# Performance work log

Hardware: AMD Instinct MI355X
Metric: run time of the kernel (lower is better)

Reference implementation:

```python
import jax, jax.numpy as jnp
import numpy as np


def setup_inputs() -> dict:
    key = jax.random.key(0)
    ks = jax.random.split(key, 12)
    B, T, S, H, I = 32, 32, 400, 1024, 1024
    s = 0.02  # weight init scale
    return {
        "input_": jax.random.normal(ks[0], (B, T, I), jnp.float32),
        "h0": jax.random.normal(ks[1], (B, H), jnp.float32),
        "c0": jax.random.normal(ks[2], (B, H), jnp.float32),
        "h_attn0": jax.random.normal(ks[3], (B, H), jnp.float32),
        "encoder_hy": jax.random.normal(ks[4], (S, B, H), jnp.float32),
        "past_attn": jax.random.uniform(ks[5], (B, S), jnp.float32),
        "W_ih": jax.random.normal(ks[6], (4 * H, I + H), jnp.float32) * s,
        "W_hh": jax.random.normal(ks[7], (4 * H, H), jnp.float32) * s,
        "b_ih": jnp.zeros((4 * H,), jnp.float32),
        "b_hh": jnp.zeros((4 * H,), jnp.float32),
        "W_attn": jax.random.normal(ks[8], (H, H), jnp.float32) * s,
        "W_out": jax.random.normal(ks[9], (H, 2 * H), jnp.float32) * s,
    }


def _decode(input_, h0, c0, h_attn0, encoder_hy, W_ih, W_hh, b_ih, b_hh, W_attn, W_out):
    # encoder_hy: [S, B, H] -> enhy: [B, S, H]
    enhy = jnp.transpose(encoder_hy, (1, 0, 2))
    # attn_in(enhy) is time-invariant (linear, fixed enhy): hoist out of the loop
    enhy_new = jnp.einsum("bsh,gh->bsg", enhy, W_attn)  # [B, S, H]
    xs = jnp.transpose(input_, (1, 0, 2))  # [T, B, I] (batch_first)

    def step(carry, x_k):
        h, c, h_attn = carry
        x = jnp.concatenate([x_k, h_attn], axis=1)  # [B, I+H]
        gates = x @ W_ih.T + b_ih + h @ W_hh.T + b_hh  # [B, 4H]
        i, f, g, o = jnp.split(gates, 4, axis=1)  # torch LSTMCell gate order
        i = jax.nn.sigmoid(i)
        f = jax.nn.sigmoid(f)
        g = jnp.tanh(g)
        o = jax.nn.sigmoid(o)
        c = f * c + i * g
        h = o * jnp.tanh(c)
        # luong_general: attn = bmm(attn_in(enhy), dehy)
        attn = jax.nn.softmax(jnp.einsum("bsh,bh->bs", enhy_new, h), axis=1)
        ctx = jnp.einsum("bs,bsh->bh", attn, enhy)
        h_attn = jnp.tanh(jnp.concatenate([ctx, h], axis=1) @ W_out.T)
        return (h, c, h_attn), (h_attn, attn)

    (h, c, h_attn), (outs, attns) = jax.lax.scan(step, (h0, c0, h_attn0), xs)
    output = jnp.transpose(outs, (1, 0, 2))  # [B, T, H] (batch_first)
    return output, h, c, h_attn, attns  # attns: [T, B, S]


def reference(input_, h0, c0, h_attn0, encoder_hy, past_attn,
              W_ih, W_hh, b_ih, b_hh, W_attn, W_out):
    output, h, c, h_attn, out_attn = _decode(
        input_, h0, c0, h_attn0, encoder_hy, W_ih, W_hh, b_ih, b_hh, W_attn, W_out)
    # coverage='none': past_attn passes through unchanged; loss_cv stays 0.0
    return output, h, c, h_attn, out_attn, past_attn, jnp.float32(0.0)
```

## Files before the change

### kernel.cpp

```cpp
#include <hip/hip_runtime.h>
#include <hip/hip_bf16.h>

using u16 = unsigned short;
typedef __attribute__((ext_vector_type(8))) short bf16x8;
typedef __attribute__((ext_vector_type(4))) float f32x4;
typedef __attribute__((ext_vector_type(4))) u16 u16x4;


__device__ __forceinline__ float bf2f(u16 u){ union{unsigned int i; float f;} v; v.i = ((unsigned int)u)<<16; return v.f; }
__device__ __forceinline__ u16 f2bf(float f){ __hip_bfloat16 h = __float2bfloat16(f); return *reinterpret_cast<u16*>(&h); }
struct HL { u16 h, l; };
__device__ __forceinline__ HL split1(float f){
  HL r; r.h = f2bf(f); r.l = f2bf(f - bf2f(r.h)); return r;
}
__device__ __forceinline__ f32x4 mfma16(bf16x8 a, bf16x8 b, f32x4 c){ return __builtin_amdgcn_mfma_f32_16x16x32_bf16(a,b,c,0,0,0); }


__global__ __launch_bounds__(256) void cast_wih_k(const float* __restrict__ Wih,
    u16* __restrict__ Wxh, u16* __restrict__ Wxl, u16* __restrict__ Wrh, u16* __restrict__ Wrl){
  int v = blockIdx.x*256 + threadIdx.x;
  if (v >= (4096*2048)/4) return;
  int flat = v*4; int j = flat >> 11; int k = flat & 2047;
  float4 f = *(const float4*)(Wih + flat);
  HL s0 = split1(f.x), s1 = split1(f.y), s2 = split1(f.z), s3 = split1(f.w);
  u16x4 h, l;
  h[0]=s0.h; h[1]=s1.h; h[2]=s2.h; h[3]=s3.h;
  l[0]=s0.l; l[1]=s1.l; l[2]=s2.l; l[3]=s3.l;
  if (k < 1024){
    *(u16x4*)(Wxh + (size_t)j*1024 + k) = h;
    *(u16x4*)(Wxl + (size_t)j*1024 + k) = l;
  } else {
    *(u16x4*)(Wrh + (size_t)j*2048 + (k-1024)) = h;
    *(u16x4*)(Wrl + (size_t)j*2048 + (k-1024)) = l;
  }
}

__global__ __launch_bounds__(256) void cast_whh_k(const float* __restrict__ Whh,
    u16* __restrict__ Wrh, u16* __restrict__ Wrl){
  int v = blockIdx.x*256 + threadIdx.x;
  if (v >= (4096*1024)/4) return;
  int flat = v*4; int j = flat >> 10; int k = flat & 1023;
  float4 f = *(const float4*)(Whh + flat);
  HL s0 = split1(f.x), s1 = split1(f.y), s2 = split1(f.z), s3 = split1(f.w);
  u16x4 h, l;
  h[0]=s0.h; h[1]=s1.h; h[2]=s2.h; h[3]=s3.h;
  l[0]=s0.l; l[1]=s1.l; l[2]=s2.l; l[3]=s3.l;
  *(u16x4*)(Wrh + (size_t)j*2048 + 1024 + k) = h;
  *(u16x4*)(Wrl + (size_t)j*2048 + 1024 + k) = l;
}

__global__ __launch_bounds__(256) void cast_split_k(const float* __restrict__ src,
    u16* __restrict__ dh, u16* __restrict__ dl, int n4){
  int v = blockIdx.x*256 + threadIdx.x;
  if (v >= n4) return;
  float4 f = *(const float4*)(src + (size_t)v*4);
  HL s0 = split1(f.x), s1 = split1(f.y), s2 = split1(f.z), s3 = split1(f.w);
  u16x4 h, l;
  h[0]=s0.h; h[1]=s1.h; h[2]=s2.h; h[3]=s3.h;
  l[0]=s0.l; l[1]=s1.l; l[2]=s2.l; l[3]=s3.l;
  *(u16x4*)(dh + (size_t)v*4) = h;
  *(u16x4*)(dl + (size_t)v*4) = l;
}

__global__ __launch_bounds__(256) void cast_x_k(const float* __restrict__ inp,
    u16* __restrict__ Xh, u16* __restrict__ Xl){
  int v = blockIdx.x*256 + threadIdx.x;
  if (v >= (1024*1024)/4) return;
  int flat = v*4; int m = flat >> 10; int k = flat & 1023;
  int t = m >> 5, b = m & 31;
  float4 f = *(const float4*)(inp + ((size_t)(b*32 + t) << 10) + k);
  HL s0 = split1(f.x), s1 = split1(f.y), s2 = split1(f.z), s3 = split1(f.w);
  u16x4 h, l;
  h[0]=s0.h; h[1]=s1.h; h[2]=s2.h; h[3]=s3.h;
  l[0]=s0.l; l[1]=s1.l; l[2]=s2.l; l[3]=s3.l;
  *(u16x4*)(Xh + flat) = h;
  *(u16x4*)(Xl + flat) = l;
}

__global__ __launch_bounds__(256) void watsplit_k(const float* __restrict__ Wattn,
    u16* __restrict__ Wth, u16* __restrict__ Wtl){
  __shared__ float t[32][33];
  int gx = blockIdx.x, cx = blockIdx.y;
  int ty = threadIdx.x >> 5, tx = threadIdx.x & 31;
  #pragma unroll
  for (int i=0;i<4;++i){
    int g = gx*32 + ty + i*8;
    t[ty+i*8][tx] = Wattn[(size_t)g*1024 + cx*32 + tx];
  }
  __syncthreads();
  #pragma unroll
  for (int i=0;i<4;++i){
    int c = cx*32 + ty + i*8;
    HL s = split1(t[tx][ty+i*8]);
    Wth[(size_t)c*1024 + gx*32 + tx] = s.h;
    Wtl[(size_t)c*1024 + gx*32 + tx] = s.l;
  }
}

__global__ __launch_bounds__(256) void init_misc_k(const float* __restrict__ h0, const float* __restrict__ c0,
    const float* __restrict__ ha0, const float* __restrict__ past,
    u16* __restrict__ Zh0, u16* __restrict__ Zl0, float* __restrict__ cbuf,
    float* __restrict__ out_past, float* __restrict__ out_loss){
  int idx = blockIdx.x*256 + threadIdx.x;
  if (idx < 65536){
    int b = idx >> 11, col = idx & 2047;
    float v = (col < 1024) ? ha0[b*1024 + col] : h0[b*1024 + col - 1024];
    HL s = split1(v);
    Zh0[idx] = s.h; Zl0[idx] = s.l;
  } else if (idx < 65536 + 32768){
    int i = idx - 65536; cbuf[i] = c0[i];
  } else if (idx < 65536 + 32768 + 12800){
    int i = idx - 98304; out_past[i] = past[i];
  } else if (idx == 65536 + 32768 + 12800){
    out_loss[0] = 0.f;
  }
}

__global__ __launch_bounds__(256) void gemm128_bias_k(
    const u16* __restrict__ Ah, const u16* __restrict__ Al,
    const u16* __restrict__ Bh, const u16* __restrict__ Bl, float* __restrict__ C,
    const float* __restrict__ bias0, const float* __restrict__ bias1, int M, int N, int K)
{
  __shared__ __align__(16) u16 Ash[4096], Asl[4096], Bsh[4096], Bsl[4096];
  const int tid = threadIdx.x;
  const int lane = tid & 63, w = tid >> 6;
  const int wm = w >> 1, wn = w & 1;
  const int m0 = blockIdx.y * 128, n0 = blockIdx.x * 128;
  const int r = lane & 15, q = lane >> 4;

  f32x4 acc[4][4];
  #pragma unroll
  for (int i=0;i<4;i++)
    #pragma unroll
    for (int j=0;j<4;j++) acc[i][j] = (f32x4){0.f,0.f,0.f,0.f};

  const int NT = K >> 5;
  const int srow = tid >> 2;
  const int skp  = (tid & 3) * 8;
  bf16x8 rah0, rah1, ral0, ral1, rbh0, rbh1, rbl0, rbl1;

  {
    size_t ao = (size_t)(m0 + srow) * K + skp;
    size_t bo = (size_t)(n0 + srow) * K + skp;
    rah0 = *(const bf16x8*)(Ah + ao);  rah1 = *(const bf16x8*)(Ah + ao + (size_t)64*K);
    ral0 = *(const bf16x8*)(Al + ao);  ral1 = *(const bf16x8*)(Al + ao + (size_t)64*K);
    rbh0 = *(const bf16x8*)(Bh + bo);  rbh1 = *(const bf16x8*)(Bh + bo + (size_t)64*K);
    rbl0 = *(const bf16x8*)(Bl + bo);  rbl1 = *(const bf16x8*)(Bl + bo + (size_t)64*K);
  }

  for (int kt = 0; kt < NT; ++kt){
    __syncthreads();
    *(bf16x8*)(Ash + tid*8)        = rah0;
    *(bf16x8*)(Ash + 2048 + tid*8) = rah1;
    *(bf16x8*)(Asl + tid*8)        = ral0;
    *(bf16x8*)(Asl + 2048 + tid*8) = ral1;
    *(bf16x8*)(Bsh + tid*8)        = rbh0;
    *(bf16x8*)(Bsh + 2048 + tid*8) = rbh1;
    *(bf16x8*)(Bsl + tid*8)        = rbl0;
    *(bf16x8*)(Bsl + 2048 + tid*8) = rbl1;
    __syncthreads();
    if (kt + 1 < NT){
      size_t ao = (size_t)(m0 + srow) * K + (kt+1)*32 + skp;
      size_t bo = (size_t)(n0 + srow) * K + (kt+1)*32 + skp;
      rah0 = *(const bf16x8*)(Ah + ao);  rah1 = *(const bf16x8*)(Ah + ao + (size_t)64*K);
      ral0 = *(const bf16x8*)(Al + ao);  ral1 = *(const bf16x8*)(Al + ao + (size_t)64*K);
      rbh0 = *(const bf16x8*)(Bh + bo);  rbh1 = *(const bf16x8*)(Bh + bo + (size_t)64*K);
      rbl0 = *(const bf16x8*)(Bl + bo);  rbl1 = *(const bf16x8*)(Bl + bo + (size_t)64*K);
    }
    bf16x8 afh[4], afl[4], bfh[4], bfl[4];
    #pragma unroll
    for (int mf=0; mf<4; ++mf){
      int off = (wm*64 + mf*16 + r)*32 + q*8;
      afh[mf] = *(const bf16x8*)(Ash + off);
      afl[mf] = *(const bf16x8*)(Asl + off);
    }
    #pragma unroll
    for (int nf=0; nf<4; ++nf){
      int off = (wn*64 + nf*16 + r)*32 + q*8;
      bfh[nf] = *(const bf16x8*)(Bsh + off);
      bfl[nf] = *(const bf16x8*)(Bsl + off);
    }
    #pragma unroll
    for (int mf=0; mf<4; ++mf)
      #pragma unroll
      for (int nf=0; nf<4; ++nf){
        acc[mf][nf] = mfma16(afh[mf], bfh[nf], acc[mf][nf]);
        acc[mf][nf] = mfma16(afh[mf], bfl[nf], acc[mf][nf]);
        acc[mf][nf] = mfma16(afl[mf], bfh[nf], acc[mf][nf]);
      }
  }

  #pragma unroll
  for (int mf=0; mf<4; ++mf)
    #pragma unroll
    for (int nf=0; nf<4; ++nf)
      #pragma unroll
      for (int rr=0; rr<4; ++rr){
        int row = m0 + wm*64 + mf*16 + q*4 + rr;
        int col = n0 + wn*64 + nf*16 + r;
        C[(size_t)row*N + col] = acc[mf][nf][rr] + bias0[col] + bias1[col];
      }
}


__global__ __launch_bounds__(512) void rec_partial_k(
    const u16* __restrict__ Zh, const u16* __restrict__ Zl,
    const u16* __restrict__ Wh, const u16* __restrict__ Wl,
    float* __restrict__ recp)
{
  __shared__ float red[8][512];
  const int tid = threadIdx.x, lane = tid & 63, w = tid >> 6;
  const int g = w & 3, kh = w >> 2;
  const int jc = blockIdx.x & 63, kq = blockIdx.x >> 6;
  const int r = lane & 15, q = lane >> 4;
  const int k0 = kq*512 + kh*256;

  f32x4 acc0 = (f32x4){0,0,0,0}, acc1 = (f32x4){0,0,0,0};
  const size_t aoff = (size_t)r*2048 + k0 + q*8;
  const size_t boff = (size_t)(g*1024 + jc*16 + r)*2048 + k0 + q*8;
  #pragma unroll
  for (int kt = 0; kt < 8; ++kt){
    bf16x8 a0h = *(const bf16x8*)(Zh + aoff + kt*32);
    bf16x8 a0l = *(const bf16x8*)(Zl + aoff + kt*32);
    bf16x8 a1h = *(const bf16x8*)(Zh + aoff + (size_t)16*2048 + kt*32);
    bf16x8 a1l = *(const bf16x8*)(Zl + aoff + (size_t)16*2048 + kt*32);
    bf16x8 bh  = *(const bf16x8*)(Wh + boff + kt*32);
    bf16x8 bl  = *(const bf16x8*)(Wl + boff + kt*32);
    acc0 = mfma16(a0h, bh, acc0);
    acc0 = mfma16(a0h, bl, acc0);
    acc0 = mfma16(a0l, bh, acc0);
    acc1 = mfma16(a1h, bh, acc1);
    acc1 = mfma16(a1h, bl, acc1);
    acc1 = mfma16(a1l, bh, acc1);
  }
  #pragma unroll
  for (int rr=0; rr<4; ++rr){
    red[w][(q*4+rr)*16 + r]      = acc0[rr];
    red[w][(16 + q*4+rr)*16 + r] = acc1[rr];
  }
  __syncthreads();
  {
    int b = tid >> 4, jj = tid & 15;
    #pragma unroll
    for (int g2=0; g2<4; ++g2){
      float v = red[g2][tid] + red[g2+4][tid];
      recp[((size_t)kq*32 + b)*4096 + g2*1024 + jc*16 + jj] = v;
    }
  }
}

__global__ __launch_bounds__(256) void cell_k(
    const float* __restrict__ recp, const float* __restrict__ gX,
    float* __restrict__ cbuf, u16* __restrict__ Znh, u16* __restrict__ Znl,
    u16* __restrict__ Zoh, u16* __restrict__ Zol,
    float* __restrict__ out_h, float* __restrict__ out_c, int last)
{
  int idx = blockIdx.x*256 + threadIdx.x;
  int b = idx >> 10, j = idx & 1023;
  float gs[4];
  #pragma unroll
  for (int g=0; g<4; ++g){
    float v = gX[(size_t)b*4096 + g*1024 + j];
    #pragma unroll
    for (int kq=0; kq<4; ++kq) v += recp[((size_t)kq*32 + b)*4096 + g*1024 + j];
    gs[g] = v;
  }
  float iv = 1.f/(1.f + expf(-gs[0]));
  float fv = 1.f/(1.f + expf(-gs[1]));
  float gv = tanhf(gs[2]);
  float ov = 1.f/(1.f + expf(-gs[3]));
  float cn = fv * cbuf[idx] + iv*gv;
  cbuf[idx] = cn;
  float h = ov * tanhf(cn);
  HL s = split1(h);
  size_t zi = (size_t)b*2048 + 1024 + j;
  Znh[zi] = s.h; Znl[zi] = s.l;
  Zoh[zi] = s.h; Zol[zi] = s.l;
  if (last){ out_h[idx] = h; out_c[idx] = cn; }
}

__global__ __launch_bounds__(512) void u_mfma_k(
    const u16* __restrict__ Zoh, const u16* __restrict__ Zol,
    const u16* __restrict__ Wth, const u16* __restrict__ Wtl,
    float* __restrict__ ubuf)
{
  __shared__ float red[8][512];
  const int tid = threadIdx.x, lane = tid & 63, w = tid >> 6;
  const int cc = blockIdx.x;
  const int r = lane & 15, q = lane >> 4;
  f32x4 acc0 = (f32x4){0,0,0,0}, acc1 = (f32x4){0,0,0,0};
  const size_t aoff = (size_t)r*2048 + 1024 + w*128 + q*8;
  const size_t boff = (size_t)(cc*16 + r)*1024 + w*128 + q*8;
  #pragma unroll
  for (int kt=0; kt<4; ++kt){
    bf16x8 a0h = *(const bf16x8*)(Zoh + aoff + kt*32);
    bf16x8 a0l = *(const bf16x8*)(Zol + aoff + kt*32);
    bf16x8 a1h = *(const bf16x8*)(Zoh + aoff + (size_t)16*2048 + kt*32);
    bf16x8 a1l = *(const bf16x8*)(Zol + aoff + (size_t)16*2048 + kt*32);
    bf16x8 bh  = *(const bf16x8*)(Wth + boff + kt*32);
    bf16x8 bl  = *(const bf16x8*)(Wtl + boff + kt*32);
    acc0 = mfma16(a0h, bh, acc0);
    acc0 = mfma16(a0h, bl, acc0);
    acc0 = mfma16(a0l, bh, acc0);
    acc1 = mfma16(a1h, bh, acc1);
    acc1 = mfma16(a1h, bl, acc1);
    acc1 = mfma16(a1l, bh, acc1);
  }
  #pragma unroll
  for (int rr=0; rr<4; ++rr){
    red[w][(q*4+rr)*16 + r]      = acc0[rr];
    red[w][(16 + q*4+rr)*16 + r] = acc1[rr];
  }
  __syncthreads();
  {
    int b = tid >> 4, jj = tid & 15;
    float v = 0.f;
    #pragma unroll
    for (int w2=0; w2<8; ++w2) v += red[w2][tid];
    ubuf[(size_t)b*1024 + cc*16 + jj] = v;
  }
}

__global__ __launch_bounds__(512) void flash_k(const float* __restrict__ enc,
    const float* __restrict__ ubuf, float* __restrict__ scbuf,
    float* __restrict__ ctxp, float* __restrict__ mlbuf)
{
  __shared__ float wacc[8][1024];
  __shared__ float wml[16];
  const int tid = threadIdx.x, lane = tid & 63, w = tid >> 6;
  const int b = blockIdx.x >> 3, sc8 = blockIdx.x & 7;
  const int s0 = sc8 * 50;

  const float* up = ubuf + (size_t)b*1024 + lane*16;
  float uu[16];
  #pragma unroll
  for (int i=0;i<4;i++){ float4 t4 = *(const float4*)(up + i*4); uu[4*i]=t4.x; uu[4*i+1]=t4.y; uu[4*i+2]=t4.z; uu[4*i+3]=t4.w; }

  float m = -1e30f, l = 0.f;
  float acc[16];
  #pragma unroll
  for (int i=0;i<16;i++) acc[i] = 0.f;

  for (int s = s0 + w; s < s0 + 50; s += 8){
    const float* ep = enc + ((size_t)s*32 + b)*1024 + lane*16;
    float er[16];
    #pragma unroll
    for (int i=0;i<4;i++){ float4 e4 = *(const float4*)(ep + i*4); er[4*i]=e4.x; er[4*i+1]=e4.y; er[4*i+2]=e4.z; er[4*i+3]=e4.w; }
    float sc = 0.f;
    #pragma unroll
    for (int i=0;i<16;i++) sc = fmaf(er[i], uu[i], sc);
    #pragma unroll
    for (int off=32; off; off>>=1) sc += __shfl_xor(sc, off);
    if (lane == 0) scbuf[(size_t)b*400 + s] = sc;
    if (sc > m){
      float f = expf(m - sc);
      l *= f;
      #pragma unroll
      for (int i=0;i<16;i++) acc[i] *= f;
      m = sc;
    }
    float wgt = expf(sc - m);
    l += wgt;
    #pragma unroll
    for (int i=0;i<16;i++) acc[i] = fmaf(wgt, er[i], acc[i]);
  }

  #pragma unroll
  for (int i=0;i<16;i++) wacc[w][lane*16+i] = acc[i];
  if (lane == 0){ wml[w*2] = m; wml[w*2+1] = l; }
  __syncthreads();

  float M = wml[0];
  #pragma unroll
  for (int i=1;i<8;i++) M = fmaxf(M, wml[i*2]);
  float c0v = 0.f, c1v = 0.f;
  #pragma unroll
  for (int i=0;i<8;i++){
    float f = expf(wml[i*2] - M);
    c0v = fmaf(wacc[i][tid],       f, c0v);
    c1v = fmaf(wacc[i][tid + 512], f, c1v);
  }
  size_t co = ((size_t)b*8 + sc8)*1024;
  ctxp[co + tid]       = c0v;
  ctxp[co + tid + 512] = c1v;
  if (tid == 0){
    float L = 0.f;
    #pragma unroll
    for (int i=0;i<8;i++) L += wml[i*2+1] * expf(wml[i*2] - M);
    mlbuf[((size_t)b*8 + sc8)*2]     = M;
    mlbuf[((size_t)b*8 + sc8)*2 + 1] = L;
  }
}

__global__ __launch_bounds__(256) void combine_k(const float* __restrict__ scbuf,
    const float* __restrict__ ctxp, const float* __restrict__ mlbuf,
    u16* __restrict__ Zoh, u16* __restrict__ Zol, float* __restrict__ attn_out)
{
  const int b = blockIdx.x >> 3, cc = blockIdx.x & 7;
  const int tid = threadIdx.x;
  float M = -1e30f;
  #pragma unroll
  for (int i=0;i<8;i++) M = fmaxf(M, mlbuf[((size_t)b*8 + i)*2]);
  float L = 0.f;
  #pragma unroll
  for (int i=0;i<8;i++) L += mlbuf[((size_t)b*8 + i)*2 + 1] * expf(mlbuf[((size_t)b*8 + i)*2] - M);
  float invL = 1.f / L;
  if (tid < 128){
    int col = cc*128 + tid;
    float v = 0.f;
    #pragma unroll
    for (int i=0;i<8;i++)
      v = fmaf(ctxp[((size_t)b*8 + i)*1024 + col], expf(mlbuf[((size_t)b*8 + i)*2] - M), v);
    HL s = split1(v * invL);
    size_t zi = (size_t)b*2048 + col;
    Zoh[zi] = s.h; Zol[zi] = s.l;
  } else if (tid < 128 + 50){
    int s = cc*50 + (tid - 128);
    attn_out[(size_t)b*400 + s] = expf(scbuf[(size_t)b*400 + s] - M) * invL;
  }
}

__global__ __launch_bounds__(512) void outg_partial_k(
    const u16* __restrict__ Zoh, const u16* __restrict__ Zol,
    const u16* __restrict__ Woh, const u16* __restrict__ Wol,
    float* __restrict__ outp)
{
  __shared__ float red[8][512];
  const int tid = threadIdx.x, lane = tid & 63, w = tid >> 6;
  const int jc = blockIdx.x & 63, kq = blockIdx.x >> 6;
  const int r = lane & 15, q = lane >> 4;
  const int k0 = kq*512 + w*64;
  f32x4 acc0 = (f32x4){0,0,0,0}, acc1 = (f32x4){0,0,0,0};
  const size_t aoff = (size_t)r*2048 + k0 + q*8;
  const size_t boff = (size_t)(jc*16 + r)*2048 + k0 + q*8;
  #pragma unroll
  for (int kt=0; kt<2; ++kt){
    bf16x8 a0h = *(const bf16x8*)(Zoh + aoff + kt*32);
    bf16x8 a0l = *(const bf16x8*)(Zol + aoff + kt*32);
    bf16x8 a1h = *(const bf16x8*)(Zoh + aoff + (size_t)16*2048 + kt*32);
    bf16x8 a1l = *(const bf16x8*)(Zol + aoff + (size_t)16*2048 + kt*32);
    bf16x8 bh  = *(const bf16x8*)(Woh + boff + kt*32);
    bf16x8 bl  = *(const bf16x8*)(Wol + boff + kt*32);
    acc0 = mfma16(a0h, bh, acc0);
    acc0 = mfma16(a0h, bl, acc0);
    acc0 = mfma16(a0l, bh, acc0);
    acc1 = mfma16(a1h, bh, acc1);
    acc1 = mfma16(a1h, bl, acc1);
    acc1 = mfma16(a1l, bh, acc1);
  }
  #pragma unroll
  for (int rr=0; rr<4; ++rr){
    red[w][(q*4+rr)*16 + r]      = acc0[rr];
    red[w][(16 + q*4+rr)*16 + r] = acc1[rr];
  }
  __syncthreads();
  {
    int b = tid >> 4, jj = tid & 15;
    float v = 0.f;
    #pragma unroll
    for (int w2=0; w2<8; ++w2) v += red[w2][tid];
    outp[((size_t)kq*32 + b)*1024 + jc*16 + jj] = v;
  }
}

__global__ __launch_bounds__(256) void outred_k(const float* __restrict__ outp,
    float* __restrict__ out_outp, u16* __restrict__ Znh, u16* __restrict__ Znl,
    float* __restrict__ out_hattn, int last)
{
  int idx = blockIdx.x*256 + threadIdx.x;
  int b = idx >> 10, uc = idx & 1023;
  float z = 0.f;
  #pragma unroll
  for (int kq=0; kq<4; ++kq) z += outp[((size_t)kq*32 + b)*1024 + uc];
  float ha = tanhf(z);
  out_outp[(size_t)b*32768 + uc] = ha;
  HL s = split1(ha);
  Znh[(size_t)b*2048 + uc] = s.h;
  Znl[(size_t)b*2048 + uc] = s.l;
  if (last) out_hattn[(size_t)b*1024 + uc] = ha;
}


extern "C" void kernel_launch(void* const* d_in, const int* in_sizes, int n_in,
                              void* d_out, int out_size, void* d_ws, size_t ws_size,
                              hipStream_t stream)
{
  const float* input_ = (const float*)d_in[0];
  const float* h0     = (const float*)d_in[1];
  const float* c0     = (const float*)d_in[2];
  const float* ha0    = (const float*)d_in[3];
  const float* enc    = (const float*)d_in[4];
  const float* past   = (const float*)d_in[5];
  const float* W_ih   = (const float*)d_in[6];
  const float* W_hh   = (const float*)d_in[7];
  const float* b_ih   = (const float*)d_in[8];
  const float* b_hh   = (const float*)d_in[9];
  const float* W_attn = (const float*)d_in[10];
  const float* W_out  = (const float*)d_in[11];
  float* out = (float*)d_out;

  const size_t OUT_OUTPUT = 0;
  const size_t OUT_H      = 1048576;
  const size_t OUT_C      = 1081344;
  const size_t OUT_HATTN  = 1114112;
  const size_t OUT_ATTN   = 1146880;
  const size_t OUT_PAST   = 1556480;
  const size_t OUT_LOSS   = 1569280;

  const size_t OFF_WRH   = 0;
  const size_t OFF_WRL   = 16777216;
  const size_t OFF_WXH   = 33554432;
  const size_t OFF_WXL   = 41943040;
  const size_t OFF_WOH   = 50331648;
  const size_t OFF_WOL   = 54525952;
  const size_t OFF_XBH   = 58720256;
  const size_t OFF_XBL   = 60817408;
  const size_t OFF_GATEX = 62914560;
  const size_t OFF_ZBH   = 79691776;
  const size_t OFF_ZBL   = 79953920;
  const size_t OFF_ZOH   = 80216064;
  const size_t OFF_ZOL   = 80347136;
  const size_t OFF_CBUF  = 80478208;
  const size_t OFF_UBUF  = 80609280;
  const size_t OFF_SC    = 80740352;
  const size_t OFF_WNORM = 80791552;
  const size_t OFF_RECP  = 80842752;
  const size_t OFF_OUTP  = 82939904;
  const size_t WS_NEED   = 83464192;
  if (ws_size < WS_NEED) return;

  const size_t OFF_CTXP  = OFF_WXH;
  const size_t OFF_ML    = OFF_WXH + 1048576;

  char* ws = (char*)d_ws;
  u16*   Wrh   = (u16*)(ws + OFF_WRH);
  u16*   Wrl   = (u16*)(ws + OFF_WRL);
  u16*   Wxh   = (u16*)(ws + OFF_WXH);
  u16*   Wxl   = (u16*)(ws + OFF_WXL);
  u16*   Woh   = (u16*)(ws + OFF_WOH);
  u16*   Wol   = (u16*)(ws + OFF_WOL);
  u16*   Xbh   = (u16*)(ws + OFF_XBH);
  u16*   Xbl   = (u16*)(ws + OFF_XBL);
  u16*   Wth   = (u16*)(ws + OFF_XBH);
  u16*   Wtl   = (u16*)(ws + OFF_XBL);
  float* gateX = (float*)(ws + OFF_GATEX);
  u16*   Zbh   = (u16*)(ws + OFF_ZBH);
  u16*   Zbl   = (u16*)(ws + OFF_ZBL);
  u16*   Zoh   = (u16*)(ws + OFF_ZOH);
  u16*   Zol   = (u16*)(ws + OFF_ZOL);
  float* cbuf  = (float*)(ws + OFF_CBUF);
  float* ubuf  = (float*)(ws + OFF_UBUF);
  float* sc    = (float*)(ws + OFF_SC);
  float* recp  = (float*)(ws + OFF_RECP);
  float* outp  = (float*)(ws + OFF_OUTP);
  float* ctxp  = (float*)(ws + OFF_CTXP);
  float* mlbuf = (float*)(ws + OFF_ML);

  cast_wih_k <<<8192, 256, 0, stream>>>(W_ih, Wxh, Wxl, Wrh, Wrl);
  cast_whh_k <<<4096, 256, 0, stream>>>(W_hh, Wrh, Wrl);
  cast_split_k<<<2048, 256, 0, stream>>>(W_out, Woh, Wol, (1024*2048)/4);
  cast_x_k   <<<1024, 256, 0, stream>>>(input_, Xbh, Xbl);
  init_misc_k<<<435, 256, 0, stream>>>(h0, c0, ha0, past, Zbh, Zbl, cbuf, out + OUT_PAST, out + OUT_LOSS);

  gemm128_bias_k<<<dim3(32, 8), 256, 0, stream>>>(Xbh, Xbl, Wxh, Wxl, gateX, b_ih, b_hh, 1024, 4096, 1024);
  watsplit_k<<<dim3(32, 32), 256, 0, stream>>>(W_attn, Wth, Wtl);

  for (int t = 0; t < 32; ++t){
    int p = t & 1;
    u16* Zih = Zbh + (size_t)p * 65536;
    u16* Zil = Zbl + (size_t)p * 65536;
    u16* Znh = Zbh + (size_t)(1-p) * 65536;
    u16* Znl = Zbl + (size_t)(1-p) * 65536;
    int last = (t == 31);
    rec_partial_k<<<256, 512, 0, stream>>>(Zih, Zil, Wrh, Wrl, recp);
    cell_k<<<128, 256, 0, stream>>>(recp, gateX + (size_t)t*131072, cbuf,
        Znh, Znl, Zoh, Zol, out + OUT_H, out + OUT_C, last);
    u_mfma_k<<<64, 512, 0, stream>>>(Zoh, Zol, Wth, Wtl, ubuf);
    flash_k<<<256, 512, 0, stream>>>(enc, ubuf, sc, ctxp, mlbuf);
    combine_k<<<256, 256, 0, stream>>>(sc, ctxp, mlbuf, Zoh, Zol,
        out + OUT_ATTN + (size_t)t*12800);
    outg_partial_k<<<256, 512, 0, stream>>>(Zoh, Zol, Woh, Wol, outp);
    outred_k<<<128, 256, 0, stream>>>(outp, out + OUT_OUTPUT + (size_t)t*1024,
        Znh, Znl, out + OUT_HATTN, last);
  }
}
```

Measured before the change: 1.400 ms.

## Overlap recurrent h-part GEMM with attention; fuse output projection and reduction

The recurrent gate GEMM is split by K. The half that depends on the new h runs inside the attention flash kernel as extra blocks, so it overlaps with attention. The h_attn half stays before the cell kernel, and a prologue launch computes the h0 half. The output projection and its tanh reduction are merged into one 64-block kernel with full K per block, which removes a launch and the partial buffer but gives much lower parallelism. The input GEMM's shared-memory rows are also padded to stride 40 to reduce bank conflicts.

```diff
diff --git a/kernel.cpp b/kernel.cpp
--- a/kernel.cpp
+++ b/kernel.cpp
@@ -116,12 +116,13 @@
   }
 }
 
+#define LDA 40
 __global__ __launch_bounds__(256) void gemm128_bias_k(
     const u16* __restrict__ Ah, const u16* __restrict__ Al,
     const u16* __restrict__ Bh, const u16* __restrict__ Bl, float* __restrict__ C,
     const float* __restrict__ bias0, const float* __restrict__ bias1, int M, int N, int K)
 {
-  __shared__ __align__(16) u16 Ash[4096], Asl[4096], Bsh[4096], Bsl[4096];
+  __shared__ __align__(16) u16 Ash[128*LDA], Asl[128*LDA], Bsh[128*LDA], Bsl[128*LDA];
   const int tid = threadIdx.x;
   const int lane = tid & 63, w = tid >> 6;
   const int wm = w >> 1, wn = w & 1;
@@ -150,14 +151,14 @@
 
   for (int kt = 0; kt < NT; ++kt){
     __syncthreads();
-    *(bf16x8*)(Ash + tid*8)        = rah0;
-    *(bf16x8*)(Ash + 2048 + tid*8) = rah1;
-    *(bf16x8*)(Asl + tid*8)        = ral0;
-    *(bf16x8*)(Asl + 2048 + tid*8) = ral1;
-    *(bf16x8*)(Bsh + tid*8)        = rbh0;
-    *(bf16x8*)(Bsh + 2048 + tid*8) = rbh1;
-    *(bf16x8*)(Bsl + tid*8)        = rbl0;
-    *(bf16x8*)(Bsl + 2048 + tid*8) = rbl1;
+    *(bf16x8*)(Ash + srow*LDA + skp)        = rah0;
+    *(bf16x8*)(Ash + (srow+64)*LDA + skp)   = rah1;
+    *(bf16x8*)(Asl + srow*LDA + skp)        = ral0;
+    *(bf16x8*)(Asl + (srow+64)*LDA + skp)   = ral1;
+    *(bf16x8*)(Bsh + srow*LDA + skp)        = rbh0;
+    *(bf16x8*)(Bsh + (srow+64)*LDA + skp)   = rbh1;
+    *(bf16x8*)(Bsl + srow*LDA + skp)        = rbl0;
+    *(bf16x8*)(Bsl + (srow+64)*LDA + skp)   = rbl1;
     __syncthreads();
     if (kt + 1 < NT){
       size_t ao = (size_t)(m0 + srow) * K + (kt+1)*32 + skp;
@@ -170,13 +171,13 @@
     bf16x8 afh[4], afl[4], bfh[4], bfl[4];
     #pragma unroll
     for (int mf=0; mf<4; ++mf){
-      int off = (wm*64 + mf*16 + r)*32 + q*8;
+      int off = (wm*64 + mf*16 + r)*LDA + q*8;
       afh[mf] = *(const bf16x8*)(Ash + off);
       afl[mf] = *(const bf16x8*)(Asl + off);
     }
     #pragma unroll
     for (int nf=0; nf<4; ++nf){
-      int off = (wn*64 + nf*16 + r)*32 + q*8;
+      int off = (wn*64 + nf*16 + r)*LDA + q*8;
       bfh[nf] = *(const bf16x8*)(Bsh + off);
       bfl[nf] = *(const bf16x8*)(Bsl + off);
     }
@@ -203,17 +204,17 @@
 }
 
 
-__global__ __launch_bounds__(512) void rec_partial_k(
+__global__ __launch_bounds__(512) void rec_slice_k(
     const u16* __restrict__ Zh, const u16* __restrict__ Zl,
     const u16* __restrict__ Wh, const u16* __restrict__ Wl,
-    float* __restrict__ recp)
+    float* __restrict__ recp, int kbase, int rbase)
 {
   __shared__ float red[8][512];
   const int tid = threadIdx.x, lane = tid & 63, w = tid >> 6;
   const int g = w & 3, kh = w >> 2;
-  const int jc = blockIdx.x & 63, kq = blockIdx.x >> 6;
+  const int jc = blockIdx.x & 63, kqq = blockIdx.x >> 6;
   const int r = lane & 15, q = lane >> 4;
-  const int k0 = kq*512 + kh*256;
+  const int k0 = kbase + kqq*512 + kh*256;
 
   f32x4 acc0 = (f32x4){0,0,0,0}, acc1 = (f32x4){0,0,0,0};
   const size_t aoff = (size_t)r*2048 + k0 + q*8;
@@ -244,7 +245,7 @@
     #pragma unroll
     for (int g2=0; g2<4; ++g2){
       float v = red[g2][tid] + red[g2+4][tid];
-      recp[((size_t)kq*32 + b)*4096 + g2*1024 + jc*16 + jj] = v;
+      recp[((size_t)(rbase+kqq)*32 + b)*4096 + g2*1024 + jc*16 + jj] = v;
     }
   }
 }
@@ -321,74 +322,120 @@
   }
 }
 
-__global__ __launch_bounds__(512) void flash_k(const float* __restrict__ enc,
+__global__ __launch_bounds__(512) void flash_rec_k(const float* __restrict__ enc,
     const float* __restrict__ ubuf, float* __restrict__ scbuf,
-    float* __restrict__ ctxp, float* __restrict__ mlbuf)
-{
-  __shared__ float wacc[8][1024];
+    float* __restrict__ ctxp, float* __restrict__ mlbuf,
+    const u16* __restrict__ Znh, const u16* __restrict__ Znl,
+    const u16* __restrict__ Wrh, const u16* __restrict__ Wrl,
+    float* __restrict__ recp)
+{
+  __shared__ __align__(16) float sm[8][1024];
   __shared__ float wml[16];
   const int tid = threadIdx.x, lane = tid & 63, w = tid >> 6;
-  const int b = blockIdx.x >> 3, sc8 = blockIdx.x & 7;
-  const int s0 = sc8 * 50;
-
-  const float* up = ubuf + (size_t)b*1024 + lane*16;
-  float uu[16];
-  #pragma unroll
-  for (int i=0;i<4;i++){ float4 t4 = *(const float4*)(up + i*4); uu[4*i]=t4.x; uu[4*i+1]=t4.y; uu[4*i+2]=t4.z; uu[4*i+3]=t4.w; }
-
-  float m = -1e30f, l = 0.f;
-  float acc[16];
-  #pragma unroll
-  for (int i=0;i<16;i++) acc[i] = 0.f;
-
-  for (int s = s0 + w; s < s0 + 50; s += 8){
-    const float* ep = enc + ((size_t)s*32 + b)*1024 + lane*16;
-    float er[16];
-    #pragma unroll
-    for (int i=0;i<4;i++){ float4 e4 = *(const float4*)(ep + i*4); er[4*i]=e4.x; er[4*i+1]=e4.y; er[4*i+2]=e4.z; er[4*i+3]=e4.w; }
-    float sc = 0.f;
-    #pragma unroll
-    for (int i=0;i<16;i++) sc = fmaf(er[i], uu[i], sc);
-    #pragma unroll
-    for (int off=32; off; off>>=1) sc += __shfl_xor(sc, off);
-    if (lane == 0) scbuf[(size_t)b*400 + s] = sc;
-    if (sc > m){
-      float f = expf(m - sc);
-      l *= f;
-      #pragma unroll
-      for (int i=0;i<16;i++) acc[i] *= f;
-      m = sc;
-    }
-    float wgt = expf(sc - m);
-    l += wgt;
-    #pragma unroll
-    for (int i=0;i<16;i++) acc[i] = fmaf(wgt, er[i], acc[i]);
-  }
-
-  #pragma unroll
-  for (int i=0;i<16;i++) wacc[w][lane*16+i] = acc[i];
-  if (lane == 0){ wml[w*2] = m; wml[w*2+1] = l; }
-  __syncthreads();
-
-  float M = wml[0];
-  #pragma unroll
-  for (int i=1;i<8;i++) M = fmaxf(M, wml[i*2]);
-  float c0v = 0.f, c1v = 0.f;
-  #pragma unroll
-  for (int i=0;i<8;i++){
-    float f = expf(wml[i*2] - M);
-    c0v = fmaf(wacc[i][tid],       f, c0v);
-    c1v = fmaf(wacc[i][tid + 512], f, c1v);
-  }
-  size_t co = ((size_t)b*8 + sc8)*1024;
-  ctxp[co + tid]       = c0v;
-  ctxp[co + tid + 512] = c1v;
-  if (tid == 0){
-    float L = 0.f;
-    #pragma unroll
-    for (int i=0;i<8;i++) L += wml[i*2+1] * expf(wml[i*2] - M);
-    mlbuf[((size_t)b*8 + sc8)*2]     = M;
-    mlbuf[((size_t)b*8 + sc8)*2 + 1] = L;
+
+  if (blockIdx.x < 256){
+    const int b = blockIdx.x >> 3, sc8 = blockIdx.x & 7;
+    const int s0 = sc8 * 50;
+
+    const float* up = ubuf + (size_t)b*1024 + lane*16;
+    float uu[16];
+    #pragma unroll
+    for (int i=0;i<4;i++){ float4 t4 = *(const float4*)(up + i*4); uu[4*i]=t4.x; uu[4*i+1]=t4.y; uu[4*i+2]=t4.z; uu[4*i+3]=t4.w; }
+
+    float m = -1e30f, l = 0.f;
+    float acc[16];
+    #pragma unroll
+    for (int i=0;i<16;i++) acc[i] = 0.f;
+
+    for (int s = s0 + w; s < s0 + 50; s += 8){
+      const float* ep = enc + ((size_t)s*32 + b)*1024 + lane*16;
+      float er[16];
+      #pragma unroll
+      for (int i=0;i<4;i++){ float4 e4 = *(const float4*)(ep + i*4); er[4*i]=e4.x; er[4*i+1]=e4.y; er[4*i+2]=e4.z; er[4*i+3]=e4.w; }
+      float sc = 0.f;
+      #pragma unroll
+      for (int i=0;i<16;i++) sc = fmaf(er[i], uu[i], sc);
+      #pragma unroll
+      for (int off=32; off; off>>=1) sc += __shfl_xor(sc, off);
+      if (lane == 0) scbuf[(size_t)b*400 + s] = sc;
+      if (sc > m){
+        float f = expf(m - sc);
+        l *= f;
+        #pragma unroll
+        for (int i=0;i<16;i++) acc[i] *= f;
+        m = sc;
+      }
+      float wgt = expf(sc - m);
+      l += wgt;
+      #pragma unroll
+      for (int i=0;i<16;i++) acc[i] = fmaf(wgt, er[i], acc[i]);
+    }
+
+    #pragma unroll
+    for (int i=0;i<16;i++) sm[w][lane*16+i] = acc[i];
+    if (lane == 0){ wml[w*2] = m; wml[w*2+1] = l; }
+    __syncthreads();
+
+    float M = wml[0];
+    #pragma unroll
+    for (int i=1;i<8;i++) M = fmaxf(M, wml[i*2]);
+    float c0v = 0.f, c1v = 0.f;
+    #pragma unroll
+    for (int i=0;i<8;i++){
+      float f = expf(wml[i*2] - M);
+      c0v = fmaf(sm[i][tid],       f, c0v);
+      c1v = fmaf(sm[i][tid + 512], f, c1v);
+    }
+    size_t co = ((size_t)b*8 + sc8)*1024;
+    ctxp[co + tid]       = c0v;
+    ctxp[co + tid + 512] = c1v;
+    if (tid == 0){
+      float L = 0.f;
+      #pragma unroll
+      for (int i=0;i<8;i++) L += wml[i*2+1] * expf(wml[i*2] - M);
+      mlbuf[((size_t)b*8 + sc8)*2]     = M;
+      mlbuf[((size_t)b*8 + sc8)*2 + 1] = L;
+    }
+  } else {
+    float (*red)[512] = (float(*)[512])sm;
+    const int bid2 = blockIdx.x - 256;
+    const int g = w & 3, kh = w >> 2;
+    const int jc = bid2 & 63, kqq = bid2 >> 6;
+    const int r = lane & 15, q = lane >> 4;
+    const int k0 = 1024 + kqq*512 + kh*256;
+
+    f32x4 acc0 = (f32x4){0,0,0,0}, acc1 = (f32x4){0,0,0,0};
+    const size_t aoff = (size_t)r*2048 + k0 + q*8;
+    const size_t boff = (size_t)(g*1024 + jc*16 + r)*2048 + k0 + q*8;
+    #pragma unroll
+    for (int kt = 0; kt < 8; ++kt){
+      bf16x8 a0h = *(const bf16x8*)(Znh + aoff + kt*32);
+      bf16x8 a0l = *(const bf16x8*)(Znl + aoff + kt*32);
+      bf16x8 a1h = *(const bf16x8*)(Znh + aoff + (size_t)16*2048 + kt*32);
+      bf16x8 a1l = *(const bf16x8*)(Znl + aoff + (size_t)16*2048 + kt*32);
+      bf16x8 bh  = *(const bf16x8*)(Wrh + boff + kt*32);
+      bf16x8 bl  = *(const bf16x8*)(Wrl + boff + kt*32);
+      acc0 = mfma16(a0h, bh, acc0);
+      acc0 = mfma16(a0h, bl, acc0);
+      acc0 = mfma16(a0l, bh, acc0);
+      acc1 = mfma16(a1h, bh, acc1);
+      acc1 = mfma16(a1h, bl, acc1);
+      acc1 = mfma16(a1l, bh, acc1);
+    }
+    #pragma unroll
+    for (int rr=0; rr<4; ++rr){
+      red[w][(q*4+rr)*16 + r]      = acc0[rr];
+      red[w][(16 + q*4+rr)*16 + r] = acc1[rr];
+    }
+    __syncthreads();
+    {
+      int b = tid >> 4, jj = tid & 15;
+      #pragma unroll
+      for (int g2=0; g2<4; ++g2){
+        float v = red[g2][tid] + red[g2+4][tid];
+        recp[((size_t)(2+kqq)*32 + b)*4096 + g2*1024 + jc*16 + jj] = v;
+      }
+    }
   }
 }
 
@@ -420,21 +467,21 @@
   }
 }
 
-__global__ __launch_bounds__(512) void outg_partial_k(
+__global__ __launch_bounds__(512) void outfull_k(
     const u16* __restrict__ Zoh, const u16* __restrict__ Zol,
     const u16* __restrict__ Woh, const u16* __restrict__ Wol,
-    float* __restrict__ outp)
+    float* __restrict__ out_outp , u16* __restrict__ Znh, u16* __restrict__ Znl,
+    float* __restrict__ out_hattn, int last)
 {
   __shared__ float red[8][512];
   const int tid = threadIdx.x, lane = tid & 63, w = tid >> 6;
-  const int jc = blockIdx.x & 63, kq = blockIdx.x >> 6;
+  const int ub = blockIdx.x;
   const int r = lane & 15, q = lane >> 4;
-  const int k0 = kq*512 + w*64;
   f32x4 acc0 = (f32x4){0,0,0,0}, acc1 = (f32x4){0,0,0,0};
-  const size_t aoff = (size_t)r*2048 + k0 + q*8;
-  const size_t boff = (size_t)(jc*16 + r)*2048 + k0 + q*8;
-  #pragma unroll
-  for (int kt=0; kt<2; ++kt){
+  const size_t aoff = (size_t)r*2048 + w*256 + q*8;
+  const size_t boff = (size_t)(ub*16 + r)*2048 + w*256 + q*8;
+  #pragma unroll
+  for (int kt=0; kt<8; ++kt){
     bf16x8 a0h = *(const bf16x8*)(Zoh + aoff + kt*32);
     bf16x8 a0l = *(const bf16x8*)(Zol + aoff + kt*32);
     bf16x8 a1h = *(const bf16x8*)(Zoh + aoff + (size_t)16*2048 + kt*32);
@@ -456,28 +503,17 @@
   __syncthreads();
   {
     int b = tid >> 4, jj = tid & 15;
-    float v = 0.f;
-    #pragma unroll
-    for (int w2=0; w2<8; ++w2) v += red[w2][tid];
-    outp[((size_t)kq*32 + b)*1024 + jc*16 + jj] = v;
-  }
-}
-
-__global__ __launch_bounds__(256) void outred_k(const float* __restrict__ outp,
-    float* __restrict__ out_outp, u16* __restrict__ Znh, u16* __restrict__ Znl,
-    float* __restrict__ out_hattn, int last)
-{
-  int idx = blockIdx.x*256 + threadIdx.x;
-  int b = idx >> 10, uc = idx & 1023;
-  float z = 0.f;
-  #pragma unroll
-  for (int kq=0; kq<4; ++kq) z += outp[((size_t)kq*32 + b)*1024 + uc];
-  float ha = tanhf(z);
-  out_outp[(size_t)b*32768 + uc] = ha;
-  HL s = split1(ha);
-  Znh[(size_t)b*2048 + uc] = s.h;
-  Znl[(size_t)b*2048 + uc] = s.l;
-  if (last) out_hattn[(size_t)b*1024 + uc] = ha;
+    int u = ub*16 + jj;
+    float z = 0.f;
+    #pragma unroll
+    for (int w2=0; w2<8; ++w2) z += red[w2][tid];
+    float ha = tanhf(z);
+    out_outp[(size_t)b*32768 + u] = ha;
+    HL s = split1(ha);
+    Znh[(size_t)b*2048 + u] = s.h;
+    Znl[(size_t)b*2048 + u] = s.l;
+    if (last) out_hattn[(size_t)b*1024 + u] = ha;
+  }
 }
 
 
@@ -523,10 +559,8 @@
   const size_t OFF_CBUF  = 80478208;
   const size_t OFF_UBUF  = 80609280;
   const size_t OFF_SC    = 80740352;
-  const size_t OFF_WNORM = 80791552;
   const size_t OFF_RECP  = 80842752;
-  const size_t OFF_OUTP  = 82939904;
-  const size_t WS_NEED   = 83464192;
+  const size_t WS_NEED   = 82939904;
   if (ws_size < WS_NEED) return;
 
   const size_t OFF_CTXP  = OFF_WXH;
@@ -552,7 +586,6 @@
   float* ubuf  = (float*)(ws + OFF_UBUF);
   float* sc    = (float*)(ws + OFF_SC);
   float* recp  = (float*)(ws + OFF_RECP);
-  float* outp  = (float*)(ws + OFF_OUTP);
   float* ctxp  = (float*)(ws + OFF_CTXP);
   float* mlbuf = (float*)(ws + OFF_ML);
 
@@ -564,6 +597,7 @@
 
   gemm128_bias_k<<<dim3(32, 8), 256, 0, stream>>>(Xbh, Xbl, Wxh, Wxl, gateX, b_ih, b_hh, 1024, 4096, 1024);
   watsplit_k<<<dim3(32, 32), 256, 0, stream>>>(W_attn, Wth, Wtl);
+  rec_slice_k<<<128, 512, 0, stream>>>(Zbh, Zbl, Wrh, Wrl, recp, 1024, 2);
 
   for (int t = 0; t < 32; ++t){
     int p = t & 1;
@@ -572,15 +606,15 @@
     u16* Znh = Zbh + (size_t)(1-p) * 65536;
     u16* Znl = Zbl + (size_t)(1-p) * 65536;
     int last = (t == 31);
-    rec_partial_k<<<256, 512, 0, stream>>>(Zih, Zil, Wrh, Wrl, recp);
+    rec_slice_k<<<128, 512, 0, stream>>>(Zih, Zil, Wrh, Wrl, recp, 0, 0);
     cell_k<<<128, 256, 0, stream>>>(recp, gateX + (size_t)t*131072, cbuf,
         Znh, Znl, Zoh, Zol, out + OUT_H, out + OUT_C, last);
     u_mfma_k<<<64, 512, 0, stream>>>(Zoh, Zol, Wth, Wtl, ubuf);
-    flash_k<<<256, 512, 0, stream>>>(enc, ubuf, sc, ctxp, mlbuf);
+    flash_rec_k<<<384, 512, 0, stream>>>(enc, ubuf, sc, ctxp, mlbuf,
+        Znh, Znl, Wrh, Wrl, recp);
     combine_k<<<256, 256, 0, stream>>>(sc, ctxp, mlbuf, Zoh, Zol,
         out + OUT_ATTN + (size_t)t*12800);
-    outg_partial_k<<<256, 512, 0, stream>>>(Zoh, Zol, Woh, Wol, outp);
-    outred_k<<<128, 256, 0, stream>>>(outp, out + OUT_OUTPUT + (size_t)t*1024,
-        Znh, Znl, out + OUT_HATTN, last);
-  }
-}
+    outfull_k<<<64, 512, 0, stream>>>(Zoh, Zol, Woh, Wol,
+        out + OUT_OUTPUT + (size_t)t*1024, Znh, Znl, out + OUT_HATTN, last);
+  }
+}
```

New measurement: 1.867 ms. 1.33x slower.

## Double split-K/S parallelism in per-step kernels and add bf16 encoder copy

Applied to the files above, without the earlier changes.

Doubles the grid of the recurrent gate GEMM, the output GEMM and the flash-attention kernel by halving each block's K or sequence range, so there are more partial sums to reduce. When the workspace is large enough, it adds a one-time bf16 cast and transpose of the encoder states into a [B,S,H] layout, so each step reads half the bytes with contiguous rows. The workspace layout is reshuffled to fit the larger partial buffers. The bf16 encoder copy drops precision in the attention scores and context, and the extra partials raise reduction work in cell_k, outred_k and combine_k.

```diff
diff --git a/kernel.cpp b/kernel.cpp
--- a/kernel.cpp
+++ b/kernel.cpp
@@ -95,6 +95,23 @@
     Wth[(size_t)c*1024 + gx*32 + tx] = s.h;
     Wtl[(size_t)c*1024 + gx*32 + tx] = s.l;
   }
+}
+
+__global__ __launch_bounds__(256) void cast_encb_k(const float* __restrict__ enc,
+    u16* __restrict__ encb){
+  int v = blockIdx.x*256 + threadIdx.x;
+  if (v >= (400*32*1024)/8) return;
+  size_t flat = (size_t)v*8;
+  int c = flat & 1023; int rem = flat >> 10;
+  int b = rem & 31, s = rem >> 5;
+  float4 f0 = *(const float4*)(enc + flat);
+  float4 f1 = *(const float4*)(enc + flat + 4);
+  u16x4 h0, h1;
+  h0[0]=f2bf(f0.x); h0[1]=f2bf(f0.y); h0[2]=f2bf(f0.z); h0[3]=f2bf(f0.w);
+  h1[0]=f2bf(f1.x); h1[1]=f2bf(f1.y); h1[2]=f2bf(f1.z); h1[3]=f2bf(f1.w);
+  u16* dst = encb + ((size_t)b*400 + s)*1024 + c;
+  *(u16x4*)dst = h0;
+  *(u16x4*)(dst+4) = h1;
 }
 
 __global__ __launch_bounds__(256) void init_misc_k(const float* __restrict__ h0, const float* __restrict__ c0,
@@ -213,13 +230,13 @@
   const int g = w & 3, kh = w >> 2;
   const int jc = blockIdx.x & 63, kq = blockIdx.x >> 6;
   const int r = lane & 15, q = lane >> 4;
-  const int k0 = kq*512 + kh*256;
+  const int k0 = kq*256 + kh*128;
 
   f32x4 acc0 = (f32x4){0,0,0,0}, acc1 = (f32x4){0,0,0,0};
   const size_t aoff = (size_t)r*2048 + k0 + q*8;
   const size_t boff = (size_t)(g*1024 + jc*16 + r)*2048 + k0 + q*8;
   #pragma unroll
-  for (int kt = 0; kt < 8; ++kt){
+  for (int kt = 0; kt < 4; ++kt){
     bf16x8 a0h = *(const bf16x8*)(Zh + aoff + kt*32);
     bf16x8 a0l = *(const bf16x8*)(Zl + aoff + kt*32);
     bf16x8 a1h = *(const bf16x8*)(Zh + aoff + (size_t)16*2048 + kt*32);
@@ -262,7 +279,7 @@
   for (int g=0; g<4; ++g){
     float v = gX[(size_t)b*4096 + g*1024 + j];
     #pragma unroll
-    for (int kq=0; kq<4; ++kq) v += recp[((size_t)kq*32 + b)*4096 + g*1024 + j];
+    for (int kq=0; kq<8; ++kq) v += recp[((size_t)kq*32 + b)*4096 + g*1024 + j];
     gs[g] = v;
   }
   float iv = 1.f/(1.f + expf(-gs[0]));
@@ -321,15 +338,15 @@
   }
 }
 
-__global__ __launch_bounds__(512) void flash_k(const float* __restrict__ enc,
+__global__ __launch_bounds__(512) void flash_bf16_k(const u16* __restrict__ encb,
     const float* __restrict__ ubuf, float* __restrict__ scbuf,
     float* __restrict__ ctxp, float* __restrict__ mlbuf)
 {
   __shared__ float wacc[8][1024];
   __shared__ float wml[16];
   const int tid = threadIdx.x, lane = tid & 63, w = tid >> 6;
-  const int b = blockIdx.x >> 3, sc8 = blockIdx.x & 7;
-  const int s0 = sc8 * 50;
+  const int b = blockIdx.x >> 4, sc16 = blockIdx.x & 15;
+  const int s0 = sc16 * 25;
 
   const float* up = ubuf + (size_t)b*1024 + lane*16;
   float uu[16];
@@ -341,11 +358,13 @@
   #pragma unroll
   for (int i=0;i<16;i++) acc[i] = 0.f;
 
-  for (int s = s0 + w; s < s0 + 50; s += 8){
-    const float* ep = enc + ((size_t)s*32 + b)*1024 + lane*16;
+  for (int s = s0 + w; s < s0 + 25; s += 8){
+    const u16* ep = encb + ((size_t)b*400 + s)*1024 + lane*16;
+    bf16x8 e0 = *(const bf16x8*)ep;
+    bf16x8 e1 = *(const bf16x8*)(ep + 8);
     float er[16];
     #pragma unroll
-    for (int i=0;i<4;i++){ float4 e4 = *(const float4*)(ep + i*4); er[4*i]=e4.x; er[4*i+1]=e4.y; er[4*i+2]=e4.z; er[4*i+3]=e4.w; }
+    for (int i=0;i<8;i++){ er[i] = bf2f((u16)e0[i]); er[8+i] = bf2f((u16)e1[i]); }
     float sc = 0.f;
     #pragma unroll
     for (int i=0;i<16;i++) sc = fmaf(er[i], uu[i], sc);
@@ -380,15 +399,86 @@
     c0v = fmaf(wacc[i][tid],       f, c0v);
     c1v = fmaf(wacc[i][tid + 512], f, c1v);
   }
-  size_t co = ((size_t)b*8 + sc8)*1024;
+  size_t co = ((size_t)b*16 + sc16)*1024;
   ctxp[co + tid]       = c0v;
   ctxp[co + tid + 512] = c1v;
   if (tid == 0){
     float L = 0.f;
     #pragma unroll
     for (int i=0;i<8;i++) L += wml[i*2+1] * expf(wml[i*2] - M);
-    mlbuf[((size_t)b*8 + sc8)*2]     = M;
-    mlbuf[((size_t)b*8 + sc8)*2 + 1] = L;
+    mlbuf[((size_t)b*16 + sc16)*2]     = M;
+    mlbuf[((size_t)b*16 + sc16)*2 + 1] = L;
+  }
+}
+
+__global__ __launch_bounds__(512) void flash_f32_k(const float* __restrict__ enc,
+    const float* __restrict__ ubuf, float* __restrict__ scbuf,
+    float* __restrict__ ctxp, float* __restrict__ mlbuf)
+{
+  __shared__ float wacc[8][1024];
+  __shared__ float wml[16];
+  const int tid = threadIdx.x, lane = tid & 63, w = tid >> 6;
+  const int b = blockIdx.x >> 4, sc16 = blockIdx.x & 15;
+  const int s0 = sc16 * 25;
+
+  const float* up = ubuf + (size_t)b*1024 + lane*16;
+  float uu[16];
+  #pragma unroll
+  for (int i=0;i<4;i++){ float4 t4 = *(const float4*)(up + i*4); uu[4*i]=t4.x; uu[4*i+1]=t4.y; uu[4*i+2]=t4.z; uu[4*i+3]=t4.w; }
+
+  float m = -1e30f, l = 0.f;
+  float acc[16];
+  #pragma unroll
+  for (int i=0;i<16;i++) acc[i] = 0.f;
+
+  for (int s = s0 + w; s < s0 + 25; s += 8){
+    const float* ep = enc + ((size_t)s*32 + b)*1024 + lane*16;
+    float er[16];
+    #pragma unroll
+    for (int i=0;i<4;i++){ float4 e4 = *(const float4*)(ep + i*4); er[4*i]=e4.x; er[4*i+1]=e4.y; er[4*i+2]=e4.z; er[4*i+3]=e4.w; }
+    float sc = 0.f;
+    #pragma unroll
+    for (int i=0;i<16;i++) sc = fmaf(er[i], uu[i], sc);
+    #pragma unroll
+    for (int off=32; off; off>>=1) sc += __shfl_xor(sc, off);
+    if (lane == 0) scbuf[(size_t)b*400 + s] = sc;
+    if (sc > m){
+      float f = expf(m - sc);
+      l *= f;
+      #pragma unroll
+      for (int i=0;i<16;i++) acc[i] *= f;
+      m = sc;
+    }
+    float wgt = expf(sc - m);
+    l += wgt;
+    #pragma unroll
+    for (int i=0;i<16;i++) acc[i] = fmaf(wgt, er[i], acc[i]);
+  }
+
+  #pragma unroll
+  for (int i=0;i<16;i++) wacc[w][lane*16+i] = acc[i];
+  if (lane == 0){ wml[w*2] = m; wml[w*2+1] = l; }
+  __syncthreads();
+
+  float M = wml[0];
+  #pragma unroll
+  for (int i=1;i<8;i++) M = fmaxf(M, wml[i*2]);
+  float c0v = 0.f, c1v = 0.f;
+  #pragma unroll
+  for (int i=0;i<8;i++){
+    float f = expf(wml[i*2] - M);
+    c0v = fmaf(wacc[i][tid],       f, c0v);
+    c1v = fmaf(wacc[i][tid + 512], f, c1v);
+  }
+  size_t co = ((size_t)b*16 + sc16)*1024;
+  ctxp[co + tid]       = c0v;
+  ctxp[co + tid + 512] = c1v;
+  if (tid == 0){
+    float L = 0.f;
+    #pragma unroll
+    for (int i=0;i<8;i++) L += wml[i*2+1] * expf(wml[i*2] - M);
+    mlbuf[((size_t)b*16 + sc16)*2]     = M;
+    mlbuf[((size_t)b*16 + sc16)*2 + 1] = L;
   }
 }
 
@@ -400,17 +490,17 @@
   const int tid = threadIdx.x;
   float M = -1e30f;
   #pragma unroll
-  for (int i=0;i<8;i++) M = fmaxf(M, mlbuf[((size_t)b*8 + i)*2]);
+  for (int i=0;i<16;i++) M = fmaxf(M, mlbuf[((size_t)b*16 + i)*2]);
   float L = 0.f;
   #pragma unroll
-  for (int i=0;i<8;i++) L += mlbuf[((size_t)b*8 + i)*2 + 1] * expf(mlbuf[((size_t)b*8 + i)*2] - M);
+  for (int i=0;i<16;i++) L += mlbuf[((size_t)b*16 + i)*2 + 1] * expf(mlbuf[((size_t)b*16 + i)*2] - M);
   float invL = 1.f / L;
   if (tid < 128){
     int col = cc*128 + tid;
     float v = 0.f;
     #pragma unroll
-    for (int i=0;i<8;i++)
-      v = fmaf(ctxp[((size_t)b*8 + i)*1024 + col], expf(mlbuf[((size_t)b*8 + i)*2] - M), v);
+    for (int i=0;i<16;i++)
+      v = fmaf(ctxp[((size_t)b*16 + i)*1024 + col], expf(mlbuf[((size_t)b*16 + i)*2] - M), v);
     HL s = split1(v * invL);
     size_t zi = (size_t)b*2048 + col;
     Zoh[zi] = s.h; Zol[zi] = s.l;
@@ -429,18 +519,17 @@
   const int tid = threadIdx.x, lane = tid & 63, w = tid >> 6;
   const int jc = blockIdx.x & 63, kq = blockIdx.x >> 6;
   const int r = lane & 15, q = lane >> 4;
-  const int k0 = kq*512 + w*64;
+  const int k0 = kq*256 + w*32;
   f32x4 acc0 = (f32x4){0,0,0,0}, acc1 = (f32x4){0,0,0,0};
   const size_t aoff = (size_t)r*2048 + k0 + q*8;
   const size_t boff = (size_t)(jc*16 + r)*2048 + k0 + q*8;
-  #pragma unroll
-  for (int kt=0; kt<2; ++kt){
-    bf16x8 a0h = *(const bf16x8*)(Zoh + aoff + kt*32);
-    bf16x8 a0l = *(const bf16x8*)(Zol + aoff + kt*32);
-    bf16x8 a1h = *(const bf16x8*)(Zoh + aoff + (size_t)16*2048 + kt*32);
-    bf16x8 a1l = *(const bf16x8*)(Zol + aoff + (size_t)16*2048 + kt*32);
-    bf16x8 bh  = *(const bf16x8*)(Woh + boff + kt*32);
-    bf16x8 bl  = *(const bf16x8*)(Wol + boff + kt*32);
+  {
+    bf16x8 a0h = *(const bf16x8*)(Zoh + aoff);
+    bf16x8 a0l = *(const bf16x8*)(Zol + aoff);
+    bf16x8 a1h = *(const bf16x8*)(Zoh + aoff + (size_t)16*2048);
+    bf16x8 a1l = *(const bf16x8*)(Zol + aoff + (size_t)16*2048);
+    bf16x8 bh  = *(const bf16x8*)(Woh + boff);
+    bf16x8 bl  = *(const bf16x8*)(Wol + boff);
     acc0 = mfma16(a0h, bh, acc0);
     acc0 = mfma16(a0h, bl, acc0);
     acc0 = mfma16(a0l, bh, acc0);
@@ -471,7 +560,7 @@
   int b = idx >> 10, uc = idx & 1023;
   float z = 0.f;
   #pragma unroll
-  for (int kq=0; kq<4; ++kq) z += outp[((size_t)kq*32 + b)*1024 + uc];
+  for (int kq=0; kq<8; ++kq) z += outp[((size_t)kq*32 + b)*1024 + uc];
   float ha = tanhf(z);
   out_outp[(size_t)b*32768 + uc] = ha;
   HL s = split1(ha);
@@ -523,14 +612,18 @@
   const size_t OFF_CBUF  = 80478208;
   const size_t OFF_UBUF  = 80609280;
   const size_t OFF_SC    = 80740352;
-  const size_t OFF_WNORM = 80791552;
-  const size_t OFF_RECP  = 80842752;
-  const size_t OFF_OUTP  = 82939904;
-  const size_t WS_NEED   = 83464192;
+  const size_t OFF_PAD   = 80842752;
+  const size_t WS_NEED   = 82939904;
   if (ws_size < WS_NEED) return;
 
+  const size_t OFF_ENCB  = WS_NEED;
+  const size_t WS_BIG    = WS_NEED + 26214400;
+  const bool use_bf16enc = (ws_size >= WS_BIG);
+
   const size_t OFF_CTXP  = OFF_WXH;
-  const size_t OFF_ML    = OFF_WXH + 1048576;
+  const size_t OFF_ML    = OFF_WXH + 2097152;
+  const size_t OFF_OUTP  = OFF_WXH + 3145728;
+  const size_t OFF_RECP  = OFF_WXL;
 
   char* ws = (char*)d_ws;
   u16*   Wrh   = (u16*)(ws + OFF_WRH);
@@ -551,16 +644,19 @@
   float* cbuf  = (float*)(ws + OFF_CBUF);
   float* ubuf  = (float*)(ws + OFF_UBUF);
   float* sc    = (float*)(ws + OFF_SC);
-  float* recp  = (float*)(ws + OFF_RECP);
-  float* outp  = (float*)(ws + OFF_OUTP);
   float* ctxp  = (float*)(ws + OFF_CTXP);
   float* mlbuf = (float*)(ws + OFF_ML);
+  float* outp  = (float*)(ws + OFF_OUTP);
+  float* recp  = (float*)(ws + OFF_RECP);
+  u16*   encb  = (u16*)(ws + OFF_ENCB);
 
   cast_wih_k <<<8192, 256, 0, stream>>>(W_ih, Wxh, Wxl, Wrh, Wrl);
   cast_whh_k <<<4096, 256, 0, stream>>>(W_hh, Wrh, Wrl);
   cast_split_k<<<2048, 256, 0, stream>>>(W_out, Woh, Wol, (1024*2048)/4);
   cast_x_k   <<<1024, 256, 0, stream>>>(input_, Xbh, Xbl);
   init_misc_k<<<435, 256, 0, stream>>>(h0, c0, ha0, past, Zbh, Zbl, cbuf, out + OUT_PAST, out + OUT_LOSS);
+  if (use_bf16enc)
+    cast_encb_k<<<6400, 256, 0, stream>>>(enc, encb);
 
   gemm128_bias_k<<<dim3(32, 8), 256, 0, stream>>>(Xbh, Xbl, Wxh, Wxl, gateX, b_ih, b_hh, 1024, 4096, 1024);
   watsplit_k<<<dim3(32, 32), 256, 0, stream>>>(W_attn, Wth, Wtl);
@@ -572,14 +668,17 @@
     u16* Znh = Zbh + (size_t)(1-p) * 65536;
     u16* Znl = Zbl + (size_t)(1-p) * 65536;
     int last = (t == 31);
-    rec_partial_k<<<256, 512, 0, stream>>>(Zih, Zil, Wrh, Wrl, recp);
+    rec_partial_k<<<512, 512, 0, stream>>>(Zih, Zil, Wrh, Wrl, recp);
     cell_k<<<128, 256, 0, stream>>>(recp, gateX + (size_t)t*131072, cbuf,
         Znh, Znl, Zoh, Zol, out + OUT_H, out + OUT_C, last);
     u_mfma_k<<<64, 512, 0, stream>>>(Zoh, Zol, Wth, Wtl, ubuf);
-    flash_k<<<256, 512, 0, stream>>>(enc, ubuf, sc, ctxp, mlbuf);
+    if (use_bf16enc)
+      flash_bf16_k<<<512, 512, 0, stream>>>(encb, ubuf, sc, ctxp, mlbuf);
+    else
+      flash_f32_k<<<512, 512, 0, stream>>>(enc, ubuf, sc, ctxp, mlbuf);
     combine_k<<<256, 256, 0, stream>>>(sc, ctxp, mlbuf, Zoh, Zol,
         out + OUT_ATTN + (size_t)t*12800);
-    outg_partial_k<<<256, 512, 0, stream>>>(Zoh, Zol, Woh, Wol, outp);
+    outg_partial_k<<<512, 512, 0, stream>>>(Zoh, Zol, Woh, Wol, outp);
     outred_k<<<128, 256, 0, stream>>>(outp, out + OUT_OUTPUT + (size_t)t*1024,
         Znh, Znl, out + OUT_HATTN, last);
   }
```

After: 1.437 ms. +2.7%, slower.
